# Kernel tuning notes

Measured on AMD Instinct MI355X. Metric: run time of the kernel, lower is better.

The kernel has to match this reference:

```python
import jax, jax.numpy as jnp
import numpy as np
import math

B, S, D, M, H = 4, 2048, 1024, 512, 8
DK = M // H


def setup_inputs() -> dict:
    key = jax.random.key(0)
    ks = jax.random.split(key, 16)
    sd = lambda fan_in: 1.0 / math.sqrt(fan_in)
    inp = {
        'x': jax.random.normal(ks[0], (B, S, D), dtype=jnp.float32),
        'W_enc': jax.random.normal(ks[1], (D, M), dtype=jnp.float32) * sd(D),
        'b_enc': jnp.zeros((M,), jnp.float32),
        'Wq': jax.random.normal(ks[2], (M, M), dtype=jnp.float32) * sd(M),
        'bq': jnp.zeros((M,), jnp.float32),
        'Wk': jax.random.normal(ks[3], (M, M), dtype=jnp.float32) * sd(M),
        'bk': jnp.zeros((M,), jnp.float32),
        'Wv': jax.random.normal(ks[4], (M, M), dtype=jnp.float32) * sd(M),
        'bv': jnp.zeros((M,), jnp.float32),
        'Wo': jax.random.normal(ks[5], (M, M), dtype=jnp.float32) * sd(M),
        'bo': jnp.zeros((M,), jnp.float32),
        'ocr_bias': jnp.zeros((1, H, 1, 1), jnp.float32),  # learned, init zeros
        'W1': jax.random.normal(ks[6], (D + M, D), dtype=jnp.float32) * sd(D + M),
        'b1': jnp.zeros((D,), jnp.float32),
        'W2': jax.random.normal(ks[7], (D, D), dtype=jnp.float32) * sd(D),
        'b2': jnp.zeros((D,), jnp.float32),
        'ln_g': jnp.ones((D,), jnp.float32),
        'ln_b': jnp.zeros((D,), jnp.float32),
    }
    return inp


def _ocr_attention(m, Wq, bq, Wk, bk, Wv, bv, Wo, bo, ocr_bias):
    b, s, _ = m.shape
    q = (m @ Wq + bq).reshape(b, s, H, DK).transpose(0, 2, 1, 3)  # bhsd
    k = (m @ Wk + bk).reshape(b, s, H, DK).transpose(0, 2, 1, 3)
    v = (m @ Wv + bv).reshape(b, s, H, DK).transpose(0, 2, 1, 3)
    scores = jnp.einsum('bhqd,bhkd->bhqk', q, k) / math.sqrt(DK) + ocr_bias
    attn = jax.nn.softmax(scores, axis=-1)  # dropout is identity at eval
    ctx = jnp.einsum('bhqk,bhkd->bhqd', attn, v)
    ctx = ctx.transpose(0, 2, 1, 3).reshape(b, s, M)
    return ctx @ Wo + bo


def _layernorm(h, g, bta, eps=1e-5):
    mu = jnp.mean(h, axis=-1, keepdims=True)
    var = jnp.mean(jnp.square(h - mu), axis=-1, keepdims=True)
    return (h - mu) * jax.lax.rsqrt(var + eps) * g + bta


def reference(x, W_enc, b_enc, Wq, bq, Wk, bk, Wv, bv, Wo, bo, ocr_bias, W1, b1, W2, b2, ln_g, ln_b):
    mem = x @ W_enc + b_enc  # [B,S,M] memory-dim stream
    attended = _ocr_attention(mem, Wq, bq, Wk, bk, Wv, bv, Wo, bo, ocr_bias)
    h = jnp.concatenate([x, attended], axis=-1) @ W1 + b1  # [B,S,D]
    h = jax.nn.gelu(h, approximate=False)
    h = h @ W2 + b2
    return _layernorm(h, ln_g, ln_b)
```

## Files before the change

kernel.cpp:

```cpp
#include <hip/hip_runtime.h>
#include <math.h>

#define B_ 4
#define S_ 2048
#define D_ 1024
#define M_ 512
#define H_ 8
#define R_ (B_ * S_)

typedef __bf16 bf8_t __attribute__((ext_vector_type(8)));
typedef __bf16 bf4_t __attribute__((ext_vector_type(4)));
typedef float f4_t __attribute__((ext_vector_type(4)));

typedef __attribute__((address_space(3))) void lds_void;
typedef const __attribute__((address_space(1))) void gl_void;
#define GL16(gp, lp) __builtin_amdgcn_global_load_lds((gl_void*)(gp), (lds_void*)(lp), 16, 0, 0)

__device__ inline unsigned packbf2(float a, float b) {
  union { __bf16 h[2]; unsigned u; } c;
  c.h[0] = (__bf16)a;
  c.h[1] = (__bf16)b;
  return c.u;
}
__device__ inline unsigned bperm(int srcBytes, unsigned v) {
  return (unsigned)__builtin_amdgcn_ds_bpermute(srcBytes, (int)v);
}

__global__ __launch_bounds__(256) void k_convert_x(const float* __restrict__ x,
                                                   __bf16* __restrict__ ab) {
  size_t i = ((size_t)blockIdx.x * 256 + threadIdx.x) * 8;
  size_t row = i >> 10;
  size_t col = i & 1023;
  f4_t f0 = *(const f4_t*)(x + i);
  f4_t f1 = *(const f4_t*)(x + i + 4);
  bf8_t v;
  v[0] = (__bf16)f0[0]; v[1] = (__bf16)f0[1]; v[2] = (__bf16)f0[2]; v[3] = (__bf16)f0[3];
  v[4] = (__bf16)f1[0]; v[5] = (__bf16)f1[1]; v[6] = (__bf16)f1[2]; v[7] = (__bf16)f1[3];
  *(bf8_t*)(ab + row * 1536 + col) = v;
}

__global__ void k_transpose(const float* __restrict__ in, __bf16* __restrict__ out,
                            int K, int N) {
  __shared__ float tile[32][33];
  const int n0 = blockIdx.x * 32;
  const int k0 = blockIdx.y * 32;
  const int tx = threadIdx.x;
  const int ty = threadIdx.y;
#pragma unroll
  for (int j = 0; j < 32; j += 8)
    tile[ty + j][tx] = in[(size_t)(k0 + ty + j) * N + n0 + tx];
  __syncthreads();
#pragma unroll
  for (int j = 0; j < 32; j += 8)
    out[(size_t)(n0 + ty + j) * K + k0 + tx] = (__bf16)tile[tx][ty + j];
}

template <int EPI>
__global__ __launch_bounds__(256) void k_gemm_bt(const __bf16* __restrict__ A, int lda,
                                                 const __bf16* __restrict__ Bt,
                                                 const float* __restrict__ bias,
                                                 __bf16* __restrict__ C, int ldc, int K) {
  __shared__ __bf16 As[128 * 32];
  __shared__ __bf16 Bs[128 * 32];
  const int t = threadIdx.x;
  const int lane = t & 63;
  const int wv = t >> 6;
  const int wr = (wv >> 1) * 64;
  const int wc = (wv & 1) * 64;
  const int bm = blockIdx.y * 128;
  const int bn = blockIdx.x * 128;
  const int c0 = wv * 2, c1 = wv * 2 + 1;
  const int sr0 = c0 * 16 + (lane >> 2);
  const int sr1 = c1 * 16 + (lane >> 2);
  const int scol = (lane & 3) * 8;
  const __bf16* Ag0 = A + (size_t)(bm + sr0) * lda + scol;
  const __bf16* Ag1 = A + (size_t)(bm + sr1) * lda + scol;
  const __bf16* Bg0 = Bt + (size_t)(bn + sr0) * (size_t)K + scol;
  const __bf16* Bg1 = Bt + (size_t)(bn + sr1) * (size_t)K + scol;
  __bf16* Al0 = As + c0 * 512;
  __bf16* Al1 = As + c1 * 512;
  __bf16* Bl0 = Bs + c0 * 512;
  __bf16* Bl1 = Bs + c1 * 512;
  f4_t acc[4][4];
#pragma unroll
  for (int m = 0; m < 4; ++m)
#pragma unroll
    for (int n = 0; n < 4; ++n) acc[m][n] = (f4_t){0.f, 0.f, 0.f, 0.f};
  const int fr = lane & 15;
  const int fk = (lane >> 4) * 8;
  for (int k0 = 0; k0 < K; k0 += 32) {
    __syncthreads();
    GL16(Ag0 + k0, Al0);
    GL16(Ag1 + k0, Al1);
    GL16(Bg0 + k0, Bl0);
    GL16(Bg1 + k0, Bl1);
    __syncthreads();
    bf8_t af[4], bfr[4];
#pragma unroll
    for (int m = 0; m < 4; ++m) af[m] = *(const bf8_t*)&As[(wr + m * 16 + fr) * 32 + fk];
#pragma unroll
    for (int n = 0; n < 4; ++n) bfr[n] = *(const bf8_t*)&Bs[(wc + n * 16 + fr) * 32 + fk];
#pragma unroll
    for (int m = 0; m < 4; ++m)
#pragma unroll
      for (int n = 0; n < 4; ++n)
        acc[m][n] = __builtin_amdgcn_mfma_f32_16x16x32_bf16(af[m], bfr[n], acc[m][n], 0, 0, 0);
  }
  const int cr = (lane >> 4) * 4;
  const int cc = lane & 15;
#pragma unroll
  for (int n = 0; n < 4; ++n) {
    const int col = bn + wc + n * 16 + cc;
    const float bv = bias[col];
#pragma unroll
    for (int m = 0; m < 4; ++m)
#pragma unroll
      for (int r = 0; r < 4; ++r) {
        const int row = bm + wr + m * 16 + cr + r;
        float v = acc[m][n][r] + bv;
        if (EPI == 1) v = 0.5f * v * (1.0f + erff(v * 0.70710678118f));
        C[(size_t)row * ldc + col] = (__bf16)v;
      }
  }
}

__global__ __launch_bounds__(256) void k_gemm_qkv(const __bf16* __restrict__ A,
                                                  const __bf16* __restrict__ Bt,
                                                  const float* __restrict__ bq,
                                                  const float* __restrict__ bk,
                                                  const float* __restrict__ bv,
                                                  __bf16* __restrict__ qb,
                                                  __bf16* __restrict__ kb,
                                                  __bf16* __restrict__ vtb) {
  const int K = 512;
  __shared__ __bf16 As[128 * 32];
  __shared__ __bf16 Bs[128 * 32];
  const int t = threadIdx.x;
  const int lane = t & 63;
  const int wv = t >> 6;
  const int wr = (wv >> 1) * 64;
  const int wc = (wv & 1) * 64;
  const int bm = blockIdx.y * 128;
  const int bn = blockIdx.x * 128;
  const int c0 = wv * 2, c1 = wv * 2 + 1;
  const int sr0 = c0 * 16 + (lane >> 2);
  const int sr1 = c1 * 16 + (lane >> 2);
  const int scol = (lane & 3) * 8;
  const __bf16* Ag0 = A + (size_t)(bm + sr0) * K + scol;
  const __bf16* Ag1 = A + (size_t)(bm + sr1) * K + scol;
  const __bf16* Bg0 = Bt + (size_t)(bn + sr0) * (size_t)K + scol;
  const __bf16* Bg1 = Bt + (size_t)(bn + sr1) * (size_t)K + scol;
  __bf16* Al0 = As + c0 * 512;
  __bf16* Al1 = As + c1 * 512;
  __bf16* Bl0 = Bs + c0 * 512;
  __bf16* Bl1 = Bs + c1 * 512;
  f4_t acc[4][4];
#pragma unroll
  for (int m = 0; m < 4; ++m)
#pragma unroll
    for (int n = 0; n < 4; ++n) acc[m][n] = (f4_t){0.f, 0.f, 0.f, 0.f};
  const int fr = lane & 15;
  const int fk = (lane >> 4) * 8;
  for (int k0 = 0; k0 < K; k0 += 32) {
    __syncthreads();
    GL16(Ag0 + k0, Al0);
    GL16(Ag1 + k0, Al1);
    GL16(Bg0 + k0, Bl0);
    GL16(Bg1 + k0, Bl1);
    __syncthreads();
    bf8_t af[4], bfr[4];
#pragma unroll
    for (int m = 0; m < 4; ++m) af[m] = *(const bf8_t*)&As[(wr + m * 16 + fr) * 32 + fk];
#pragma unroll
    for (int n = 0; n < 4; ++n) bfr[n] = *(const bf8_t*)&Bs[(wc + n * 16 + fr) * 32 + fk];
#pragma unroll
    for (int m = 0; m < 4; ++m)
#pragma unroll
      for (int n = 0; n < 4; ++n)
        acc[m][n] = __builtin_amdgcn_mfma_f32_16x16x32_bf16(af[m], bfr[n], acc[m][n], 0, 0, 0);
  }
  const int cr = (lane >> 4) * 4;
  const int cc = lane & 15;
  const int seg = bn >> 9;
  const float* bsel = (seg == 0) ? bq : (seg == 1) ? bk : bv;
  if (seg < 2) {
    __bf16* dst = (seg == 0) ? qb : kb;
#pragma unroll
    for (int n = 0; n < 4; ++n) {
      const int col = (bn + wc + n * 16 + cc) & 511;
      const float bvv = bsel[col];
#pragma unroll
      for (int m = 0; m < 4; ++m)
#pragma unroll
        for (int r = 0; r < 4; ++r) {
          const int row = bm + wr + m * 16 + cr + r;
          dst[(size_t)row * 512 + col] = (__bf16)(acc[m][n][r] + bvv);
        }
    }
  } else {
#pragma unroll
    for (int n = 0; n < 4; ++n) {
      const int col = (bn + wc + n * 16 + cc) & 511;
      const float bvv = bsel[col];
#pragma unroll
      for (int m = 0; m < 4; ++m) {
        const int rb = bm + wr + m * 16 + cr;
        bf4_t w;
#pragma unroll
        for (int r = 0; r < 4; ++r) w[r] = (__bf16)(acc[m][n][r] + bvv);
        *(bf4_t*)(vtb + ((size_t)((rb >> 11) * 512 + col)) * 2048 + (rb & 2047)) = w;
      }
    }
  }
}

__global__ __launch_bounds__(256, 2) void k_attn3(const __bf16* __restrict__ qb,
                                                  const __bf16* __restrict__ kb,
                                                  const __bf16* __restrict__ vt,
                                                  __bf16* __restrict__ ctx) {
  const int t = threadIdx.x;
  const int lane = t & 63;
  const int wv = t >> 6;
  const int i = blockIdx.x;
  const int xcd = i & 7;
  const int jj = i >> 3;
  const int bh = xcd + 8 * (jj & 3);
  const int xt = jj >> 2;
  const int b = bh >> 3, h = bh & 7;
  const int q0 = xt * 128 + wv * 32;
  const int fr = lane & 15;
  const int g = lane >> 4;
  const int fk = g * 8;
  const float qs = 0.125f * 1.44269504f;
  bf8_t bqf[2][2];
#pragma unroll
  for (int tt = 0; tt < 2; ++tt)
#pragma unroll
    for (int s = 0; s < 2; ++s) {
      bf8_t raw = *(const bf8_t*)(qb + ((size_t)b * S_ + q0 + tt * 16 + fr) * M_ + h * 64 + s * 32 + fk);
      bf8_t sc;
#pragma unroll
      for (int e = 0; e < 8; ++e) sc[e] = (__bf16)((float)raw[e] * qs);
      bqf[tt][s] = sc;
    }
  const __bf16* kbase = kb + (size_t)b * S_ * M_ + h * 64;
  const __bf16* vbase = vt + ((size_t)(b * 512 + h * 64)) * (size_t)S_;
  float mreg[2] = {-3e38f, -3e38f};
  float lreg[2] = {0.f, 0.f};
  f4_t o[2][4];
#pragma unroll
  for (int tt = 0; tt < 2; ++tt)
#pragma unroll
    for (int d = 0; d < 4; ++d) o[tt][d] = (f4_t){0.f, 0.f, 0.f, 0.f};
  const int srcA = (fr + ((g & 1) << 5)) << 2;
  const int srcB = srcA + 64;
  bf8_t ak0[4][2], ak1[4][2];
#pragma unroll
  for (int hh = 0; hh < 4; ++hh)
#pragma unroll
    for (int s = 0; s < 2; ++s)
      ak0[hh][s] = *(const bf8_t*)(kbase + (size_t)(hh * 16 + fr) * M_ + s * 32 + fk);

#define ATTN_CHUNK(AKC, AKN, KV)                                                          \
  {                                                                                       \
    bf8_t bvf[2][4];                                                                      \
    _Pragma("unroll") for (int ks = 0; ks < 2; ++ks)                                      \
        _Pragma("unroll") for (int d = 0; d < 4; ++d)                                     \
            bvf[ks][d] = *(const bf8_t*)(vbase + (size_t)(d * 16 + fr) * S_ + (KV) + ks * 32 + fk); \
    f4_t st[2][4];                                                                        \
    __builtin_amdgcn_s_setprio(1);                                                        \
    _Pragma("unroll") for (int tt = 0; tt < 2; ++tt)                                      \
        _Pragma("unroll") for (int hh = 0; hh < 4; ++hh) {                                \
      f4_t a = (f4_t){0.f, 0.f, 0.f, 0.f};                                                \
      a = __builtin_amdgcn_mfma_f32_16x16x32_bf16(AKC[hh][0], bqf[tt][0], a, 0, 0, 0);    \
      a = __builtin_amdgcn_mfma_f32_16x16x32_bf16(AKC[hh][1], bqf[tt][1], a, 0, 0, 0);    \
      st[tt][hh] = a;                                                                     \
    }                                                                                     \
    __builtin_amdgcn_s_setprio(0);                                                        \
    const int kvn = ((KV) + 64) & (S_ - 1);                                               \
    _Pragma("unroll") for (int hh = 0; hh < 4; ++hh)                                      \
        _Pragma("unroll") for (int s = 0; s < 2; ++s)                                     \
            AKN[hh][s] = *(const bf8_t*)(kbase + (size_t)(kvn + hh * 16 + fr) * M_ + s * 32 + fk); \
    _Pragma("unroll") for (int tt = 0; tt < 2; ++tt) {                                    \
      float pm = -3e38f;                                                                  \
      _Pragma("unroll") for (int hh = 0; hh < 4; ++hh)                                    \
          _Pragma("unroll") for (int r = 0; r < 4; ++r) pm = fmaxf(pm, st[tt][hh][r]);    \
      pm = fmaxf(pm, __shfl_xor(pm, 16, 64));                                             \
      pm = fmaxf(pm, __shfl_xor(pm, 32, 64));                                             \
      float mo = mreg[tt];                                                                \
      if (!__all(pm <= mo + 8.f)) {                                                       \
        const float mn = fmaxf(mo, pm);                                                   \
        const float al = exp2f(mo - mn);                                                  \
        mreg[tt] = mn;                                                                    \
        mo = mn;                                                                          \
        lreg[tt] *= al;                                                                   \
        float alr[4];                                                                     \
        _Pragma("unroll") for (int r = 0; r < 4; ++r) alr[r] = __shfl(al, g * 4 + r, 64); \
        _Pragma("unroll") for (int d = 0; d < 4; ++d)                                     \
            _Pragma("unroll") for (int r = 0; r < 4; ++r) o[tt][d][r] *= alr[r];          \
      }                                                                                   \
      float p[4][4];                                                                      \
      float ps = 0.f;                                                                     \
      _Pragma("unroll") for (int hh = 0; hh < 4; ++hh)                                    \
          _Pragma("unroll") for (int r = 0; r < 4; ++r) {                                 \
        p[hh][r] = exp2f(st[tt][hh][r] - mo);                                             \
        ps += p[hh][r];                                                                   \
      }                                                                                   \
      ps += __shfl_xor(ps, 16, 64);                                                       \
      ps += __shfl_xor(ps, 32, 64);                                                       \
      lreg[tt] += ps;                                                                     \
      union { unsigned u[4]; bf8_t v; } aw[2];                                            \
      _Pragma("unroll") for (int ks = 0; ks < 2; ++ks) {                                  \
        unsigned ch0 = packbf2(p[2 * ks][0], p[2 * ks][1]);                               \
        unsigned ch1 = packbf2(p[2 * ks][2], p[2 * ks][3]);                               \
        unsigned ch2 = packbf2(p[2 * ks + 1][0], p[2 * ks + 1][1]);                       \
        unsigned ch3 = packbf2(p[2 * ks + 1][2], p[2 * ks + 1][3]);                       \
        unsigned t0 = bperm(srcA, ch0), t2 = bperm(srcA, ch2);                            \
        unsigned t1 = bperm(srcA, ch1), t3 = bperm(srcA, ch3);                            \
        unsigned u0 = bperm(srcB, ch0), u2 = bperm(srcB, ch2);                            \
        unsigned u1 = bperm(srcB, ch1), u3 = bperm(srcB, ch3);                            \
        const bool lo = (g < 2);                                                          \
        aw[ks].u[0] = lo ? t0 : t2;                                                       \
        aw[ks].u[1] = lo ? t1 : t3;                                                       \
        aw[ks].u[2] = lo ? u0 : u2;                                                       \
        aw[ks].u[3] = lo ? u1 : u3;                                                       \
      }                                                                                   \
      __builtin_amdgcn_s_setprio(1);                                                      \
      _Pragma("unroll") for (int d = 0; d < 4; ++d) {                                     \
        o[tt][d] = __builtin_amdgcn_mfma_f32_16x16x32_bf16(aw[0].v, bvf[0][d], o[tt][d], 0, 0, 0); \
        o[tt][d] = __builtin_amdgcn_mfma_f32_16x16x32_bf16(aw[1].v, bvf[1][d], o[tt][d], 0, 0, 0); \
      }                                                                                   \
      __builtin_amdgcn_s_setprio(0);                                                      \
    }                                                                                     \
  }

  for (int kv = 0; kv < S_; kv += 128) {
    ATTN_CHUNK(ak0, ak1, kv);
    ATTN_CHUNK(ak1, ak0, kv + 64);
  }
#undef ATTN_CHUNK

#pragma unroll
  for (int tt = 0; tt < 2; ++tt) {
    float lrr[4];
#pragma unroll
    for (int r = 0; r < 4; ++r) lrr[r] = __shfl(lreg[tt], g * 4 + r, 64);
#pragma unroll
    for (int d = 0; d < 4; ++d)
#pragma unroll
      for (int r = 0; r < 4; ++r) {
        const float v = o[tt][d][r] / lrr[r];
        ctx[((size_t)b * S_ + q0 + tt * 16 + g * 4 + r) * M_ + h * 64 + d * 16 + fr] = (__bf16)v;
      }
  }
}

__global__ __launch_bounds__(256) void k_ln(const __bf16* __restrict__ hh,
                                            const float* __restrict__ g,
                                            const float* __restrict__ bt,
                                            float* __restrict__ out) {
  const int row = blockIdx.x;
  const int t = threadIdx.x;
  const __bf16* hp = hh + (size_t)row * 1024 + t * 4;
  bf4_t v = *(const bf4_t*)hp;
  float f[4];
  float s1 = 0.f, s2 = 0.f;
#pragma unroll
  for (int j = 0; j < 4; ++j) {
    f[j] = (float)v[j];
    s1 += f[j];
    s2 += f[j] * f[j];
  }
#pragma unroll
  for (int d = 1; d < 64; d <<= 1) {
    s1 += __shfl_xor(s1, d, 64);
    s2 += __shfl_xor(s2, d, 64);
  }
  __shared__ float red[8];
  const int lane = t & 63, wv = t >> 6;
  if (lane == 0) { red[wv] = s1; red[4 + wv] = s2; }
  __syncthreads();
  const float S1 = red[0] + red[1] + red[2] + red[3];
  const float S2 = red[4] + red[5] + red[6] + red[7];
  const float mu = S1 * (1.f / 1024.f);
  const float var = S2 * (1.f / 1024.f) - mu * mu;
  const float inv = rsqrtf(var + 1e-5f);
  float* op = out + (size_t)row * 1024 + t * 4;
#pragma unroll
  for (int j = 0; j < 4; ++j) op[j] = (f[j] - mu) * inv * g[t * 4 + j] + bt[t * 4 + j];
}

extern "C" void kernel_launch(void* const* d_in, const int* in_sizes, int n_in,
                              void* d_out, int out_size, void* d_ws, size_t ws_size,
                              hipStream_t stream) {
  const float* x = (const float*)d_in[0];
  const float* W_enc = (const float*)d_in[1];
  const float* b_enc = (const float*)d_in[2];
  const float* Wq = (const float*)d_in[3];
  const float* bq = (const float*)d_in[4];
  const float* Wk = (const float*)d_in[5];
  const float* bk = (const float*)d_in[6];
  const float* Wv = (const float*)d_in[7];
  const float* bv = (const float*)d_in[8];
  const float* Wo = (const float*)d_in[9];
  const float* bo = (const float*)d_in[10];
  const float* W1 = (const float*)d_in[12];
  const float* b1 = (const float*)d_in[13];
  const float* W2 = (const float*)d_in[14];
  const float* b2 = (const float*)d_in[15];
  const float* lng = (const float*)d_in[16];
  const float* lnb = (const float*)d_in[17];
  float* out = (float*)d_out;

  __bf16* p = (__bf16*)d_ws;
  __bf16* ab = p;  p += (size_t)R_ * 1536;
  __bf16* mem = p; p += (size_t)R_ * 512;
  __bf16* qb = p;  p += (size_t)R_ * 512;
  __bf16* kb = p;  p += (size_t)R_ * 512;
  __bf16* vtb = p; p += (size_t)R_ * 512;
  __bf16* cx = p;  p += (size_t)R_ * 512;
  __bf16* h1 = p;  p += (size_t)R_ * 1024;
  __bf16* h2 = p;  p += (size_t)R_ * 1024;
  __bf16* WtE = p; p += (size_t)512 * 1024;
  __bf16* WtQ = p; p += (size_t)512 * 512;
  __bf16* WtK = p; p += (size_t)512 * 512;
  __bf16* WtV = p; p += (size_t)512 * 512;
  __bf16* WtO = p; p += (size_t)512 * 512;
  __bf16* Wt1 = p; p += (size_t)1024 * 1536;
  __bf16* Wt2 = p; p += (size_t)1024 * 1024;

  k_convert_x<<<4096, 256, 0, stream>>>(x, ab);
  dim3 tb(32, 8);
  k_transpose<<<dim3(16, 32), tb, 0, stream>>>(W_enc, WtE, 1024, 512);
  k_transpose<<<dim3(16, 16), tb, 0, stream>>>(Wq, WtQ, 512, 512);
  k_transpose<<<dim3(16, 16), tb, 0, stream>>>(Wk, WtK, 512, 512);
  k_transpose<<<dim3(16, 16), tb, 0, stream>>>(Wv, WtV, 512, 512);
  k_transpose<<<dim3(16, 16), tb, 0, stream>>>(Wo, WtO, 512, 512);
  k_transpose<<<dim3(32, 48), tb, 0, stream>>>(W1, Wt1, 1536, 1024);
  k_transpose<<<dim3(32, 32), tb, 0, stream>>>(W2, Wt2, 1024, 1024);
  k_gemm_bt<0><<<dim3(4, 64), 256, 0, stream>>>(ab, 1536, WtE, b_enc, mem, 512, 1024);
  k_gemm_qkv<<<dim3(12, 64), 256, 0, stream>>>(mem, WtQ, bq, bk, bv, qb, kb, vtb);
  k_attn3<<<512, 256, 0, stream>>>(qb, kb, vtb, cx);
  k_gemm_bt<0><<<dim3(4, 64), 256, 0, stream>>>(cx, 512, WtO, bo, ab + 1024, 1536, 512);
  k_gemm_bt<1><<<dim3(8, 64), 256, 0, stream>>>(ab, 1536, Wt1, b1, h1, 1024, 1536);
  k_gemm_bt<0><<<dim3(8, 64), 256, 0, stream>>>(h1, 1024, Wt2, b2, h2, 1024, 1024);
  k_ln<<<R_, 256, 0, stream>>>(h2, lng, lnb, out);
}
```

Baseline: 413.6 us.

## Pre-pack K/V into MFMA fragment order and stage attention tiles via LDS

The QKV GEMM epilogue now writes K and V in a packed layout that matches the MFMA fragment order. The attention kernel streams 128-key chunks of that layout into LDS with global_load_lds, replacing per-lane strided global loads and the register double-buffering of K. Separately, the eight weight-transpose and x-convert launches are merged into one k_prep kernel to cut launch overhead. Risks: the K/V epilogue stores become scattered, and the attention loop now has two block barriers per chunk and no overlap between staging and compute.

```diff
diff --git a/kernel.cpp b/kernel.cpp
--- a/kernel.cpp
+++ b/kernel.cpp
@@ -26,33 +26,48 @@
   return (unsigned)__builtin_amdgcn_ds_bpermute(srcBytes, (int)v);
 }
 
-__global__ __launch_bounds__(256) void k_convert_x(const float* __restrict__ x,
-                                                   __bf16* __restrict__ ab) {
-  size_t i = ((size_t)blockIdx.x * 256 + threadIdx.x) * 8;
-  size_t row = i >> 10;
-  size_t col = i & 1023;
-  f4_t f0 = *(const f4_t*)(x + i);
-  f4_t f1 = *(const f4_t*)(x + i + 4);
-  bf8_t v;
-  v[0] = (__bf16)f0[0]; v[1] = (__bf16)f0[1]; v[2] = (__bf16)f0[2]; v[3] = (__bf16)f0[3];
-  v[4] = (__bf16)f1[0]; v[5] = (__bf16)f1[1]; v[6] = (__bf16)f1[2]; v[7] = (__bf16)f1[3];
-  *(bf8_t*)(ab + row * 1536 + col) = v;
-}
-
-__global__ void k_transpose(const float* __restrict__ in, __bf16* __restrict__ out,
-                            int K, int N) {
-  __shared__ float tile[32][33];
-  const int n0 = blockIdx.x * 32;
-  const int k0 = blockIdx.y * 32;
-  const int tx = threadIdx.x;
-  const int ty = threadIdx.y;
-#pragma unroll
-  for (int j = 0; j < 32; j += 8)
-    tile[ty + j][tx] = in[(size_t)(k0 + ty + j) * N + n0 + tx];
-  __syncthreads();
-#pragma unroll
-  for (int j = 0; j < 32; j += 8)
-    out[(size_t)(n0 + ty + j) * K + k0 + tx] = (__bf16)tile[tx][ty + j];
+struct PrepArgs {
+  const float* src[7];
+  __bf16* dst[7];
+  int K[7], N[7];
+  int start[8];
+  const float* x;
+  __bf16* ab;
+};
+
+__global__ __launch_bounds__(256) void k_prep(PrepArgs a) {
+  const int t = threadIdx.x;
+  const int id = blockIdx.x;
+  if (id < a.start[7]) {
+    int w = 0;
+    while (id >= a.start[w + 1]) ++w;
+    const int local = id - a.start[w];
+    const int bxw = a.N[w] >> 5;
+    const int n0 = (local % bxw) * 32;
+    const int k0 = (local / bxw) * 32;
+    const int tx = t & 31, ty = t >> 5;
+    __shared__ float tile[32][33];
+    const float* in = a.src[w];
+    __bf16* out = a.dst[w];
+    const int N = a.N[w], K = a.K[w];
+#pragma unroll
+    for (int j = 0; j < 32; j += 8)
+      tile[ty + j][tx] = in[(size_t)(k0 + ty + j) * N + n0 + tx];
+    __syncthreads();
+#pragma unroll
+    for (int j = 0; j < 32; j += 8)
+      out[(size_t)(n0 + ty + j) * K + k0 + tx] = (__bf16)tile[tx][ty + j];
+  } else {
+    size_t i = (((size_t)(id - a.start[7])) * 256 + t) * 8;
+    size_t row = i >> 10;
+    size_t col = i & 1023;
+    f4_t f0 = *(const f4_t*)(a.x + i);
+    f4_t f1 = *(const f4_t*)(a.x + i + 4);
+    bf8_t v;
+    v[0] = (__bf16)f0[0]; v[1] = (__bf16)f0[1]; v[2] = (__bf16)f0[2]; v[3] = (__bf16)f0[3];
+    v[4] = (__bf16)f1[0]; v[5] = (__bf16)f1[1]; v[6] = (__bf16)f1[2]; v[7] = (__bf16)f1[3];
+    *(bf8_t*)(a.ab + row * 1536 + col) = v;
+  }
 }
 
 template <int EPI>
@@ -128,10 +143,10 @@
                                                   const __bf16* __restrict__ Bt,
                                                   const float* __restrict__ bq,
                                                   const float* __restrict__ bk,
-                                                  const float* __restrict__ bv,
+                                                  const float* __restrict__ bvb,
                                                   __bf16* __restrict__ qb,
-                                                  __bf16* __restrict__ kb,
-                                                  __bf16* __restrict__ vtb) {
+                                                  __bf16* __restrict__ pkd,
+                                                  __bf16* __restrict__ pvd) {
   const int K = 512;
   __shared__ __bf16 As[128 * 32];
   __shared__ __bf16 Bs[128 * 32];
@@ -182,42 +197,64 @@
   const int cr = (lane >> 4) * 4;
   const int cc = lane & 15;
   const int seg = bn >> 9;
-  const float* bsel = (seg == 0) ? bq : (seg == 1) ? bk : bv;
-  if (seg < 2) {
-    __bf16* dst = (seg == 0) ? qb : kb;
+  const int b0 = bm >> 11;
+  if (seg == 0) {
 #pragma unroll
     for (int n = 0; n < 4; ++n) {
       const int col = (bn + wc + n * 16 + cc) & 511;
-      const float bvv = bsel[col];
+      const float bvv = bq[col];
 #pragma unroll
       for (int m = 0; m < 4; ++m)
 #pragma unroll
         for (int r = 0; r < 4; ++r) {
           const int row = bm + wr + m * 16 + cr + r;
-          dst[(size_t)row * 512 + col] = (__bf16)(acc[m][n][r] + bvv);
+          qb[(size_t)row * 512 + col] = (__bf16)(acc[m][n][r] + bvv);
+        }
+    }
+  } else if (seg == 1) {
+#pragma unroll
+    for (int n = 0; n < 4; ++n) {
+      const int col = (bn + wc + n * 16 + cc) & 511;
+      const int hh = col >> 6, d = col & 63;
+      const int s = d >> 5, g2 = (d >> 3) & 3, e = d & 7;
+      const float bvv = bk[col];
+#pragma unroll
+      for (int m = 0; m < 4; ++m)
+#pragma unroll
+        for (int r = 0; r < 4; ++r) {
+          const int key = (bm + wr + m * 16 + cr + r) & 2047;
+          const int k16 = key >> 4, frk = key & 15;
+          pkd[(((size_t)(b0 * 8 + hh) * 128 + k16) * 2 + s) * 512 + (g2 * 16 + frk) * 8 + e] =
+              (__bf16)(acc[m][n][r] + bvv);
         }
     }
   } else {
 #pragma unroll
     for (int n = 0; n < 4; ++n) {
       const int col = (bn + wc + n * 16 + cc) & 511;
-      const float bvv = bsel[col];
+      const int hh = col >> 6, dd = col & 63;
+      const int d16 = dd >> 4, fv = dd & 15;
+      const float bvv = bvb[col];
 #pragma unroll
       for (int m = 0; m < 4; ++m) {
-        const int rb = bm + wr + m * 16 + cr;
+        const int keyb = (bm + wr + m * 16 + cr) & 2047;
+        const int kc = keyb >> 6, ks = (keyb >> 5) & 1, g2 = (keyb >> 3) & 3, e0 = keyb & 7;
         bf4_t w;
 #pragma unroll
         for (int r = 0; r < 4; ++r) w[r] = (__bf16)(acc[m][n][r] + bvv);
-        *(bf4_t*)(vtb + ((size_t)((rb >> 11) * 512 + col)) * 2048 + (rb & 2047)) = w;
+        *(bf4_t*)&pvd[((((size_t)(b0 * 8 + hh) * 32 + kc) * 2 + ks) * 4 + d16) * 512 +
+                      (g2 * 16 + fv) * 8 + e0] = w;
       }
     }
   }
 }
 
-__global__ __launch_bounds__(256, 2) void k_attn3(const __bf16* __restrict__ qb,
-                                                  const __bf16* __restrict__ kb,
-                                                  const __bf16* __restrict__ vt,
+__global__ __launch_bounds__(256, 2) void k_attn4(const __bf16* __restrict__ qb,
+                                                  const __bf16* __restrict__ pk,
+                                                  const __bf16* __restrict__ pv,
                                                   __bf16* __restrict__ ctx) {
+  __shared__ __bf16 KL[8192];
+  __shared__ __bf16 VL[8192];
   const int t = threadIdx.x;
   const int lane = t & 63;
   const int wv = t >> 6;
@@ -243,8 +280,8 @@
       for (int e = 0; e < 8; ++e) sc[e] = (__bf16)((float)raw[e] * qs);
       bqf[tt][s] = sc;
     }
-  const __bf16* kbase = kb + (size_t)b * S_ * M_ + h * 64;
-  const __bf16* vbase = vt + ((size_t)(b * 512 + h * 64)) * (size_t)S_;
+  const __bf16* pkc = pk + (size_t)bh * 131072;
+  const __bf16* pvc = pv + (size_t)bh * 131072;
   float mreg[2] = {-3e38f, -3e38f};
   float lreg[2] = {0.f, 0.f};
   f4_t o[2][4];
@@ -254,33 +291,35 @@
     for (int d = 0; d < 4; ++d) o[tt][d] = (f4_t){0.f, 0.f, 0.f, 0.f};
   const int srcA = (fr + ((g & 1) << 5)) << 2;
   const int srcB = srcA + 64;
-  bf8_t ak0[4][2], ak1[4][2];
-#pragma unroll
-  for (int hh = 0; hh < 4; ++hh)
-#pragma unroll
-    for (int s = 0; s < 2; ++s)
-      ak0[hh][s] = *(const bf8_t*)(kbase + (size_t)(hh * 16 + fr) * M_ + s * 32 + fk);
-
-#define ATTN_CHUNK(AKC, AKN, KV)                                                          \
+
+#define STAGE(KV)                                                                      \
+  {                                                                                    \
+    const size_t goff = (size_t)(KV) * 64;                                             \
+    _Pragma("unroll") for (int j = 0; j < 4; ++j) {                                    \
+      GL16(pkc + goff + (wv * 4 + j) * 512 + lane * 8, KL + (wv * 4 + j) * 512);       \
+      GL16(pvc + goff + (wv * 4 + j) * 512 + lane * 8, VL + (wv * 4 + j) * 512);       \
+    }                                                                                  \
+  }
+
+#define COMPUTE64(HALF)                                                                   \
   {                                                                                       \
-    bf8_t bvf[2][4];                                                                      \
+    bf8_t ak[4][2], bvf[2][4];                                                            \
+    _Pragma("unroll") for (int hh = 0; hh < 4; ++hh)                                      \
+        _Pragma("unroll") for (int s = 0; s < 2; ++s)                                     \
+            ak[hh][s] = *(const bf8_t*)&KL[(HALF) * 4096 + (hh * 2 + s) * 512 + lane * 8];\
     _Pragma("unroll") for (int ks = 0; ks < 2; ++ks)                                      \
         _Pragma("unroll") for (int d = 0; d < 4; ++d)                                     \
-            bvf[ks][d] = *(const bf8_t*)(vbase + (size_t)(d * 16 + fr) * S_ + (KV) + ks * 32 + fk); \
+            bvf[ks][d] = *(const bf8_t*)&VL[(HALF) * 4096 + (ks * 4 + d) * 512 + lane * 8];\
     f4_t st[2][4];                                                                        \
     __builtin_amdgcn_s_setprio(1);                                                        \
     _Pragma("unroll") for (int tt = 0; tt < 2; ++tt)                                      \
         _Pragma("unroll") for (int hh = 0; hh < 4; ++hh) {                                \
       f4_t a = (f4_t){0.f, 0.f, 0.f, 0.f};                                                \
-      a = __builtin_amdgcn_mfma_f32_16x16x32_bf16(AKC[hh][0], bqf[tt][0], a, 0, 0, 0);    \
-      a = __builtin_amdgcn_mfma_f32_16x16x32_bf16(AKC[hh][1], bqf[tt][1], a, 0, 0, 0);    \
+      a = __builtin_amdgcn_mfma_f32_16x16x32_bf16(ak[hh][0], bqf[tt][0], a, 0, 0, 0);     \
+      a = __builtin_amdgcn_mfma_f32_16x16x32_bf16(ak[hh][1], bqf[tt][1], a, 0, 0, 0);     \
       st[tt][hh] = a;                                                                     \
     }                                                                                     \
     __builtin_amdgcn_s_setprio(0);                                                        \
-    const int kvn = ((KV) + 64) & (S_ - 1);                                               \
-    _Pragma("unroll") for (int hh = 0; hh < 4; ++hh)                                      \
-        _Pragma("unroll") for (int s = 0; s < 2; ++s)                                     \
-            AKN[hh][s] = *(const bf8_t*)(kbase + (size_t)(kvn + hh * 16 + fr) * M_ + s * 32 + fk); \
     _Pragma("unroll") for (int tt = 0; tt < 2; ++tt) {                                    \
       float pm = -3e38f;                                                                  \
       _Pragma("unroll") for (int hh = 0; hh < 4; ++hh)                                    \
@@ -334,11 +373,16 @@
     }                                                                                     \
   }
 
+  STAGE(0);
   for (int kv = 0; kv < S_; kv += 128) {
-    ATTN_CHUNK(ak0, ak1, kv);
-    ATTN_CHUNK(ak1, ak0, kv + 64);
-  }
-#undef ATTN_CHUNK
+    __syncthreads();
+    COMPUTE64(0);
+    COMPUTE64(1);
+    __syncthreads();
+    if (kv + 128 < S_) STAGE(kv + 128);
+  }
+#undef STAGE
+#undef COMPUTE64
 
 #pragma unroll
   for (int tt = 0; tt < 2; ++tt) {
@@ -416,8 +460,8 @@
   __bf16* ab = p;  p += (size_t)R_ * 1536;
   __bf16* mem = p; p += (size_t)R_ * 512;
   __bf16* qb = p;  p += (size_t)R_ * 512;
-  __bf16* kb = p;  p += (size_t)R_ * 512;
-  __bf16* vtb = p; p += (size_t)R_ * 512;
+  __bf16* pk = p;  p += (size_t)R_ * 512;
+  __bf16* pv = p;  p += (size_t)R_ * 512;
   __bf16* cx = p;  p += (size_t)R_ * 512;
   __bf16* h1 = p;  p += (size_t)R_ * 1024;
   __bf16* h2 = p;  p += (size_t)R_ * 1024;
@@ -429,18 +473,25 @@
   __bf16* Wt1 = p; p += (size_t)1024 * 1536;
   __bf16* Wt2 = p; p += (size_t)1024 * 1024;
 
-  k_convert_x<<<4096, 256, 0, stream>>>(x, ab);
-  dim3 tb(32, 8);
-  k_transpose<<<dim3(16, 32), tb, 0, stream>>>(W_enc, WtE, 1024, 512);
-  k_transpose<<<dim3(16, 16), tb, 0, stream>>>(Wq, WtQ, 512, 512);
-  k_transpose<<<dim3(16, 16), tb, 0, stream>>>(Wk, WtK, 512, 512);
-  k_transpose<<<dim3(16, 16), tb, 0, stream>>>(Wv, WtV, 512, 512);
-  k_transpose<<<dim3(16, 16), tb, 0, stream>>>(Wo, WtO, 512, 512);
-  k_transpose<<<dim3(32, 48), tb, 0, stream>>>(W1, Wt1, 1536, 1024);
-  k_transpose<<<dim3(32, 32), tb, 0, stream>>>(W2, Wt2, 1024, 1024);
+  PrepArgs pa;
+  pa.src[0] = W_enc; pa.dst[0] = WtE; pa.K[0] = 1024; pa.N[0] = 512;
+  pa.src[1] = Wq;    pa.dst[1] = WtQ; pa.K[1] = 512;  pa.N[1] = 512;
+  pa.src[2] = Wk;    pa.dst[2] = WtK; pa.K[2] = 512;  pa.N[2] = 512;
+  pa.src[3] = Wv;    pa.dst[3] = WtV; pa.K[3] = 512;  pa.N[3] = 512;
+  pa.src[4] = Wo;    pa.dst[4] = WtO; pa.K[4] = 512;  pa.N[4] = 512;
+  pa.src[5] = W1;    pa.dst[5] = Wt1; pa.K[5] = 1536; pa.N[5] = 1024;
+  pa.src[6] = W2;    pa.dst[6] = Wt2; pa.K[6] = 1024; pa.N[6] = 1024;
+  int acc0 = 0;
+  for (int w = 0; w < 7; ++w) {
+    pa.start[w] = acc0;
+    acc0 += (pa.N[w] >> 5) * (pa.K[w] >> 5);
+  }
+  pa.start[7] = acc0;
+  pa.x = x; pa.ab = ab;
+  k_prep<<<acc0 + 4096, 256, 0, stream>>>(pa);
   k_gemm_bt<0><<<dim3(4, 64), 256, 0, stream>>>(ab, 1536, WtE, b_enc, mem, 512, 1024);
-  k_gemm_qkv<<<dim3(12, 64), 256, 0, stream>>>(mem, WtQ, bq, bk, bv, qb, kb, vtb);
-  k_attn3<<<512, 256, 0, stream>>>(qb, kb, vtb, cx);
+  k_gemm_qkv<<<dim3(12, 64), 256, 0, stream>>>(mem, WtQ, bq, bk, bv, qb, pk, pv);
+  k_attn4<<<512, 256, 0, stream>>>(qb, pk, pv, cx);
   k_gemm_bt<0><<<dim3(4, 64), 256, 0, stream>>>(cx, 512, WtO, bo, ab + 1024, 1536, 512);
   k_gemm_bt<1><<<dim3(8, 64), 256, 0, stream>>>(ab, 1536, Wt1, b1, h1, 1024, 1536);
   k_gemm_bt<0><<<dim3(8, 64), 256, 0, stream>>>(h1, 1024, Wt2, b2, h2, 1024, 1024);
```

After: 370.1 us. 10.5% less time.
